# Performance work log

Measured on AMD Instinct MI355X. Metric: run time of the kernel, lower is better.

Reference implementation:

```python
import jax, jax.numpy as jnp
import numpy as np

B, N, K_OUT, NBASIS, NGLOBALS, H = 16, 2048, 128, 4, 2, 256
DIN = 1 + NBASIS + N + NGLOBALS  # norm + basis projections + all-pairs dots + globals
NEG_SLOPE = 0.01  # torch LeakyReLU default


def setup_inputs() -> dict:
    key = jax.random.key(0)
    ks = jax.random.split(key, 6)
    x = jax.random.uniform(ks[0], (B, N, 3), jnp.float32)      # positions -> dots >= 0
    u = jax.random.normal(ks[1], (B, NGLOBALS), jnp.float32)
    basis = jax.random.normal(ks[2], (B, NBASIS, 3), jnp.float32)
    def init_w(k, fan_in, fan_out):
        return jax.random.normal(k, (fan_in, fan_out), jnp.float32) / np.float32(np.sqrt(fan_in))
    W1 = init_w(ks[3], DIN, H); b1 = jnp.zeros((H,), jnp.float32)
    W2 = init_w(ks[4], H, H);   b2 = jnp.zeros((H,), jnp.float32)
    W3 = init_w(ks[5], H, K_OUT); b3 = jnp.zeros((K_OUT,), jnp.float32)
    return {"x": x, "u": u, "basis": basis,
            "W1": W1, "b1": b1, "W2": W2, "b2": b2, "W3": W3, "b3": b3}


def reference(x, u, basis, W1, b1, W2, b2, W3, b3):
    # per-vector norms: [B, N, 1]
    norms = jnp.linalg.norm(x, axis=-1, keepdims=True)
    # projections onto basis vectors: [B, N, NBASIS]
    proj = jnp.einsum('bid,bnd->bin', x, basis)
    # all-pairs sqrt of dot products: [B, N, N]
    dots = jnp.sqrt(jnp.einsum('bid,bjd->bij', x, x))
    # concat order matches original: globals first, then [norm, proj, dots]
    u_rep = jnp.broadcast_to(u[:, None, :], (B, N, NGLOBALS))
    scalars = jnp.concatenate([u_rep, norms, proj, dots], axis=-1)  # [B, N, DIN]
    # MLP (Linear -> LeakyReLU -> Linear -> LeakyReLU -> Linear)
    h = jax.nn.leaky_relu(scalars @ W1 + b1, NEG_SLOPE)
    h = jax.nn.leaky_relu(h @ W2 + b2, NEG_SLOPE)
    fk = h @ W3 + b3  # [B, N, K_OUT]
    # outer product with x followed by mean over input vecs, fused into one einsum
    # (avoids materializing the [B, N, K_OUT, 3] tensor)
    return jnp.einsum('bio,bid->bod', fk, x) / np.float32(N)  # [B, K_OUT, 3]
```

## Files before the change

kernel.cpp:

```cpp
#include <hip/hip_runtime.h>

typedef unsigned short u16;
typedef unsigned int   u32;

typedef __attribute__((ext_vector_type(8))) short short8;
typedef __attribute__((ext_vector_type(4))) float floatx4;

__device__ __forceinline__ u16 f2bf(float f) {
    u32 u = __float_as_uint(f);
    u = u + 0x7fffu + ((u >> 16) & 1u);
    return (u16)(u >> 16);
}

__device__ __forceinline__ u32 pack2bf(float s0, float s1) {
    u32 a = __float_as_uint(s0) + 0x8000u;
    u32 b = __float_as_uint(s1) + 0x8000u;
    return __builtin_amdgcn_perm(b, a, 0x07060302u);
}

__device__ __forceinline__ floatx4 mfma16(short8 a, short8 b, floatx4 c) {
    return __builtin_amdgcn_mfma_f32_16x16x32_bf16(a, b, c, 0, 0, 0);
}

__global__ void k_prep(const float* __restrict__ W1, const float* __restrict__ W2,
                       const float* __restrict__ W3, u16* __restrict__ W1frag,
                       u16* __restrict__ W2T, u16* __restrict__ W3T) {
    int idx = blockIdx.x * 256 + threadIdx.x;
    if (idx < 524288) {
        int kt = idx >> 13, r = idx & 8191;
        int t = r >> 5, jj = (r >> 3) & 3, ji = r & 7;
        int lane = t & 63, wv = t >> 6, lr = lane & 15, lq = lane >> 4;
        int n = wv * 64 + jj * 16 + lr;
        int k = kt * 32 + lq * 8 + ji;
        W1frag[idx] = f2bf(W1[(7 + k) * 256 + n]);
    } else if (idx < 589824) {
        int i = idx - 524288;
        int n = i >> 8, k = i & 255;
        W2T[i] = f2bf(W2[k * 256 + n]);
    } else if (idx < 622592) {
        int i = idx - 589824;
        int n = i >> 8, k = i & 255;
        W3T[i] = f2bf(W3[k * 128 + n]);
    }
}

__global__ __launch_bounds__(256, 2) void k_h1(
    const float* __restrict__ x, const float* __restrict__ u,
    const float* __restrict__ basis, const float* __restrict__ W1,
    const float* __restrict__ b1, const u16* __restrict__ W1frag,
    u16* __restrict__ h1) {
    __shared__ float4 xls4[1536];
    __shared__ u16 As[2][64][40];
    __shared__ float rowsml[64][6];
    __shared__ float colsml[256][6];

    const int t = threadIdx.x;
    const int b = blockIdx.y;
    const int i0 = blockIdx.x * 64;
    const int lane = t & 63, wv = t >> 6;
    const int lr = lane & 15, lq = lane >> 4;
    float* xls = (float*)xls4;

    {
        const float4* src = (const float4*)(x + b * 6144);
#pragma unroll
        for (int i = 0; i < 6; ++i) xls4[t + i * 256] = src[t + i * 256];
    }
    {
        int c = t;
        float u0 = u[b * 2 + 0], u1 = u[b * 2 + 1];
        colsml[c][0] = b1[c] + u0 * W1[c] + u1 * W1[256 + c];
        colsml[c][1] = W1[512 + c];
        colsml[c][2] = W1[768 + c];
        colsml[c][3] = W1[1024 + c];
        colsml[c][4] = W1[1280 + c];
        colsml[c][5] = W1[1536 + c];
    }
    __syncthreads();
    if (t < 64) {
        float xx = xls[(i0 + t) * 3], xy = xls[(i0 + t) * 3 + 1], xz = xls[(i0 + t) * 3 + 2];
        rowsml[t][0] = sqrtf(xx * xx + xy * xy + xz * xz);
#pragma unroll
        for (int p = 0; p < 4; ++p) {
            const float* bp = basis + (b * 4 + p) * 3;
            rowsml[t][1 + p] = xx * bp[0] + xy * bp[1] + xz * bp[2];
        }
    }
    const float ax = xls[(i0 + lane) * 3];
    const float ay = xls[(i0 + lane) * 3 + 1];
    const float az = xls[(i0 + lane) * 3 + 2];
    const int cbase = wv * 8;
    const u16* wf = W1frag + t * 32;

    auto gen_store = [&](int kt, int buf) {
        int q = kt * 24 + wv * 6;
        float4 q0 = xls4[q], q1 = xls4[q + 1], q2 = xls4[q + 2];
        float4 q3 = xls4[q + 3], q4 = xls4[q + 4], q5 = xls4[q + 5];
        float s0 = __builtin_amdgcn_sqrtf(ax * q0.x + ay * q0.y + az * q0.z);
        float s1 = __builtin_amdgcn_sqrtf(ax * q0.w + ay * q1.x + az * q1.y);
        float s2 = __builtin_amdgcn_sqrtf(ax * q1.z + ay * q1.w + az * q2.x);
        float s3 = __builtin_amdgcn_sqrtf(ax * q2.y + ay * q2.z + az * q2.w);
        float s4 = __builtin_amdgcn_sqrtf(ax * q3.x + ay * q3.y + az * q3.z);
        float s5 = __builtin_amdgcn_sqrtf(ax * q3.w + ay * q4.x + az * q4.y);
        float s6 = __builtin_amdgcn_sqrtf(ax * q4.z + ay * q4.w + az * q5.x);
        float s7 = __builtin_amdgcn_sqrtf(ax * q5.y + ay * q5.z + az * q5.w);
        uint4 dv;
        dv.x = pack2bf(s0, s1); dv.y = pack2bf(s2, s3);
        dv.z = pack2bf(s4, s5); dv.w = pack2bf(s6, s7);
        *(uint4*)&As[buf][lane][cbase] = dv;
    };

    floatx4 acc[4][4];
    const floatx4 zero = {0.f, 0.f, 0.f, 0.f};
#pragma unroll
    for (int i = 0; i < 4; ++i)
#pragma unroll
        for (int j = 0; j < 4; ++j) acc[i][j] = zero;

    short8 acur[4], bcur[4], bnxt[4];
    gen_store(0, 0);
#pragma unroll
    for (int j = 0; j < 4; ++j) bcur[j] = *(const short8*)(wf + j * 8);
    __syncthreads();
#pragma unroll
    for (int i = 0; i < 4; ++i) acur[i] = *(const short8*)&As[0][i * 16 + lr][lq * 8];

#pragma unroll 2
    for (int kt = 0; kt < 64; ++kt) {
        if (kt < 63) {
            const u16* wn = wf + (kt + 1) * 8192;
#pragma unroll
            for (int j = 0; j < 4; ++j) bnxt[j] = *(const short8*)(wn + j * 8);
            gen_store(kt + 1, (kt + 1) & 1);
        }
#pragma unroll
        for (int i = 0; i < 4; ++i)
#pragma unroll
            for (int j = 0; j < 4; ++j)
                acc[i][j] = mfma16(acur[i], bcur[j], acc[i][j]);
        __syncthreads();
        if (kt < 63) {
#pragma unroll
            for (int i = 0; i < 4; ++i)
                acur[i] = *(const short8*)&As[(kt + 1) & 1][i * 16 + lr][lq * 8];
#pragma unroll
            for (int j = 0; j < 4; ++j) bcur[j] = bnxt[j];
        }
    }

#pragma unroll
    for (int i = 0; i < 4; ++i) {
#pragma unroll
        for (int r = 0; r < 4; ++r) {
            int row = i * 16 + lq * 4 + r;
            float nrm = rowsml[row][0];
            float p0 = rowsml[row][1], p1 = rowsml[row][2];
            float p2 = rowsml[row][3], p3 = rowsml[row][4];
            u16* orow = h1 + (b * 2048 + i0 + row) * 256;
#pragma unroll
            for (int j = 0; j < 4; ++j) {
                int col = wv * 64 + j * 16 + lr;
                float v = acc[i][j][r] + colsml[col][0] + nrm * colsml[col][1] +
                          p0 * colsml[col][2] + p1 * colsml[col][3] +
                          p2 * colsml[col][4] + p3 * colsml[col][5];
                v = v > 0.f ? v : 0.01f * v;
                orow[col] = f2bf(v);
            }
        }
    }
}

__global__ __launch_bounds__(256, 2) void k_tail(
    const u16* __restrict__ h1, const u16* __restrict__ W2T,
    const float* __restrict__ b2, const u16* __restrict__ W3T,
    const float* __restrict__ b3, const float* __restrict__ x,
    float* __restrict__ accum) {
    __shared__ u16 As[64][40];
    __shared__ u16 Bs[256][40];
    __shared__ u16 h2s[64][264];
    __shared__ float colb2[256];
    __shared__ float colb3[128];
    __shared__ float xs[64][4];
    __shared__ float red[128][4];

    const int t = threadIdx.x;
    const int m0 = blockIdx.x * 64;
    const int b = m0 >> 11, i0 = m0 & 2047;
    const int lane = t & 63, wv = t >> 6;
    const int lr = lane & 15, lq = lane >> 4;

    colb2[t] = b2[t];
    if (t < 128) colb3[t] = b3[t];
    if (t < 64) {
        const float* xp = x + (b * 2048 + i0 + t) * 3;
        xs[t][0] = xp[0]; xs[t][1] = xp[1]; xs[t][2] = xp[2];
    }

    floatx4 acc[4][4];
    const floatx4 zero = {0.f, 0.f, 0.f, 0.f};
#pragma unroll
    for (int i = 0; i < 4; ++i)
#pragma unroll
        for (int j = 0; j < 4; ++j) acc[i][j] = zero;

    const int ar = t >> 2, ac = (t & 3) * 8;
    for (int kt = 0; kt < 8; ++kt) {
        *(uint4*)&As[ar][ac] = *(const uint4*)(h1 + (m0 + ar) * 256 + kt * 32 + ac);
        const u16* wsrc = W2T + t * 256 + kt * 32;
        *(uint4*)&Bs[t][0]  = *(const uint4*)(wsrc);
        *(uint4*)&Bs[t][8]  = *(const uint4*)(wsrc + 8);
        *(uint4*)&Bs[t][16] = *(const uint4*)(wsrc + 16);
        *(uint4*)&Bs[t][24] = *(const uint4*)(wsrc + 24);
        __syncthreads();
        short8 af[4], bf[4];
#pragma unroll
        for (int i = 0; i < 4; ++i) af[i] = *(const short8*)&As[i * 16 + lr][lq * 8];
#pragma unroll
        for (int j = 0; j < 4; ++j) bf[j] = *(const short8*)&Bs[wv * 64 + j * 16 + lr][lq * 8];
#pragma unroll
        for (int i = 0; i < 4; ++i)
#pragma unroll
            for (int j = 0; j < 4; ++j) acc[i][j] = mfma16(af[i], bf[j], acc[i][j]);
        __syncthreads();
    }
#pragma unroll
    for (int i = 0; i < 4; ++i)
#pragma unroll
        for (int r = 0; r < 4; ++r) {
            int row = i * 16 + lq * 4 + r;
#pragma unroll
            for (int j = 0; j < 4; ++j) {
                int col = wv * 64 + j * 16 + lr;
                float v = acc[i][j][r] + colb2[col];
                v = v > 0.f ? v : 0.01f * v;
                h2s[row][col] = f2bf(v);
            }
        }
    __syncthreads();

    floatx4 acc2[4][2];
#pragma unroll
    for (int i = 0; i < 4; ++i)
#pragma unroll
        for (int j = 0; j < 2; ++j) acc2[i][j] = zero;

    u16 (*Ws)[40] = (u16(*)[40])Bs;
    const int wr = t & 127, wseg = (t >> 7) * 16;
    for (int kt = 0; kt < 8; ++kt) {
        const u16* w3src = W3T + wr * 256 + kt * 32 + wseg;
        *(uint4*)&Ws[wr][wseg]     = *(const uint4*)(w3src);
        *(uint4*)&Ws[wr][wseg + 8] = *(const uint4*)(w3src + 8);
        __syncthreads();
        short8 af[4], bf[2];
#pragma unroll
        for (int i = 0; i < 4; ++i) af[i] = *(const short8*)&h2s[i * 16 + lr][kt * 32 + lq * 8];
#pragma unroll
        for (int j = 0; j < 2; ++j) bf[j] = *(const short8*)&Ws[wv * 32 + j * 16 + lr][lq * 8];
#pragma unroll
        for (int i = 0; i < 4; ++i)
#pragma unroll
            for (int j = 0; j < 2; ++j) acc2[i][j] = mfma16(af[i], bf[j], acc2[i][j]);
        __syncthreads();
    }

    float s[2][3];
#pragma unroll
    for (int j = 0; j < 2; ++j) { s[j][0] = 0.f; s[j][1] = 0.f; s[j][2] = 0.f; }
#pragma unroll
    for (int i = 0; i < 4; ++i)
#pragma unroll
        for (int r = 0; r < 4; ++r) {
            int row = i * 16 + lq * 4 + r;
            float x0 = xs[row][0], x1 = xs[row][1], x2 = xs[row][2];
#pragma unroll
            for (int j = 0; j < 2; ++j) {
                int col = wv * 32 + j * 16 + lr;
                float fk = acc2[i][j][r] + colb3[col];
                s[j][0] += fk * x0; s[j][1] += fk * x1; s[j][2] += fk * x2;
            }
        }
#pragma unroll
    for (int j = 0; j < 2; ++j)
#pragma unroll
        for (int d = 0; d < 3; ++d) {
            float v = s[j][d];
            v += __shfl_xor(v, 16);
            v += __shfl_xor(v, 32);
            if (lane < 16) red[wv * 32 + j * 16 + lane][d] = v;
        }
    __syncthreads();
    if (t < 128) {
#pragma unroll
        for (int d = 0; d < 3; ++d)
            atomicAdd(&accum[(b * 128 + t) * 3 + d], red[t][d]);
    }
}

__global__ void k_fin(const float* __restrict__ accum, float* __restrict__ out) {
    int idx = blockIdx.x * 256 + threadIdx.x;
    if (idx < 6144) out[idx] = accum[idx] * (1.0f / 2048.0f);
}

extern "C" void kernel_launch(void* const* d_in, const int* in_sizes, int n_in,
                              void* d_out, int out_size, void* d_ws, size_t ws_size,
                              hipStream_t stream) {
    const float* x     = (const float*)d_in[0];
    const float* u     = (const float*)d_in[1];
    const float* basis = (const float*)d_in[2];
    const float* W1    = (const float*)d_in[3];
    const float* b1    = (const float*)d_in[4];
    const float* W2    = (const float*)d_in[5];
    const float* b2    = (const float*)d_in[6];
    const float* W3    = (const float*)d_in[7];
    const float* b3    = (const float*)d_in[8];
    float* out = (float*)d_out;

    char* ws = (char*)d_ws;
    u16*  W1frag = (u16*)ws;
    u16*  W2T    = (u16*)(ws + 1048576);
    u16*  W3T    = (u16*)(ws + 1179648);
    u16*  h1     = (u16*)(ws + 1245184);
    float* accum = (float*)(ws + 18022400);

    hipMemsetAsync(accum, 0, 24576, stream);
    k_prep<<<2432, 256, 0, stream>>>(W1, W2, W3, W1frag, W2T, W3T);
    k_h1<<<dim3(32, 16), 256, 0, stream>>>(x, u, basis, W1, b1, W1frag, h1);
    k_tail<<<512, 256, 0, stream>>>(h1, W2T, b2, W3T, b3, x, accum);
    k_fin<<<24, 256, 0, stream>>>(accum, out);
}
```

Measured before the change: 145.0 us.

## Widen h1 to 8 waves with SoA x, fragment-packed W2/W3 loads in tail

Result: no change. 143.6 us (-1.0%).

```diff
diff --git a/kernel.cpp b/kernel.cpp
--- a/kernel.cpp
+++ b/kernel.cpp
@@ -5,6 +5,7 @@
 
 typedef __attribute__((ext_vector_type(8))) short short8;
 typedef __attribute__((ext_vector_type(4))) float floatx4;
+typedef __attribute__((ext_vector_type(2))) float v2f;
 
 __device__ __forceinline__ u16 f2bf(float f) {
     u32 u = __float_as_uint(f);
@@ -24,32 +25,34 @@
 
 __global__ void k_prep(const float* __restrict__ W1, const float* __restrict__ W2,
                        const float* __restrict__ W3, u16* __restrict__ W1frag,
-                       u16* __restrict__ W2T, u16* __restrict__ W3T) {
+                       u16* __restrict__ W2frag, u16* __restrict__ W3frag) {
     int idx = blockIdx.x * 256 + threadIdx.x;
     if (idx < 524288) {
         int kt = idx >> 13, r = idx & 8191;
+        int t = r >> 4, j = (r >> 3) & 1, ji = r & 7;
+        int lane = t & 63, w = t >> 6, lr = lane & 15, lq = lane >> 4;
+        W1frag[idx] = f2bf(W1[(7 + kt * 32 + lq * 8 + ji) * 256 + w * 32 + j * 16 + lr]);
+    } else if (idx < 589824) {
+        int i = idx - 524288;
+        int kt = i >> 13, r = i & 8191;
         int t = r >> 5, jj = (r >> 3) & 3, ji = r & 7;
         int lane = t & 63, wv = t >> 6, lr = lane & 15, lq = lane >> 4;
-        int n = wv * 64 + jj * 16 + lr;
-        int k = kt * 32 + lq * 8 + ji;
-        W1frag[idx] = f2bf(W1[(7 + k) * 256 + n]);
-    } else if (idx < 589824) {
-        int i = idx - 524288;
-        int n = i >> 8, k = i & 255;
-        W2T[i] = f2bf(W2[k * 256 + n]);
+        W2frag[i] = f2bf(W2[(kt * 32 + lq * 8 + ji) * 256 + wv * 64 + jj * 16 + lr]);
     } else if (idx < 622592) {
         int i = idx - 589824;
-        int n = i >> 8, k = i & 255;
-        W3T[i] = f2bf(W3[k * 128 + n]);
-    }
-}
-
-__global__ __launch_bounds__(256, 2) void k_h1(
+        int kt = i >> 12, r = i & 4095;
+        int t = r >> 4, j = (r >> 3) & 1, ji = r & 7;
+        int lane = t & 63, wv = t >> 6, lr = lane & 15, lq = lane >> 4;
+        W3frag[i] = f2bf(W3[(kt * 32 + lq * 8 + ji) * 128 + wv * 32 + j * 16 + lr]);
+    }
+}
+
+__global__ __launch_bounds__(512, 4) void k_h1(
     const float* __restrict__ x, const float* __restrict__ u,
     const float* __restrict__ basis, const float* __restrict__ W1,
     const float* __restrict__ b1, const u16* __restrict__ W1frag,
     u16* __restrict__ h1) {
-    __shared__ float4 xls4[1536];
+    __shared__ float xls[6144];
     __shared__ u16 As[2][64][40];
     __shared__ float rowsml[64][6];
     __shared__ float colsml[256][6];
@@ -57,16 +60,25 @@
     const int t = threadIdx.x;
     const int b = blockIdx.y;
     const int i0 = blockIdx.x * 64;
-    const int lane = t & 63, wv = t >> 6;
+    const int lane = t & 63, w = t >> 6;
     const int lr = lane & 15, lq = lane >> 4;
-    float* xls = (float*)xls4;
 
     {
         const float4* src = (const float4*)(x + b * 6144);
 #pragma unroll
-        for (int i = 0; i < 6; ++i) xls4[t + i * 256] = src[t + i * 256];
-    }
-    {
+        for (int kk = 0; kk < 3; ++kk) {
+            int q = t + kk * 512;
+            float4 v = src[q];
+            float vv[4] = {v.x, v.y, v.z, v.w};
+            int e = q * 4;
+#pragma unroll
+            for (int cc = 0; cc < 4; ++cc) {
+                int ee = e + cc;
+                xls[(ee % 3) * 2048 + ee / 3] = vv[cc];
+            }
+        }
+    }
+    if (t < 256) {
         int c = t;
         float u0 = u[b * 2 + 0], u1 = u[b * 2 + 1];
         colsml[c][0] = b1[c] + u0 * W1[c] + u1 * W1[256 + c];
@@ -78,7 +90,7 @@
     }
     __syncthreads();
     if (t < 64) {
-        float xx = xls[(i0 + t) * 3], xy = xls[(i0 + t) * 3 + 1], xz = xls[(i0 + t) * 3 + 2];
+        float xx = xls[i0 + t], xy = xls[2048 + i0 + t], xz = xls[4096 + i0 + t];
         rowsml[t][0] = sqrtf(xx * xx + xy * xy + xz * xz);
 #pragma unroll
         for (int p = 0; p < 4; ++p) {
@@ -86,41 +98,40 @@
             rowsml[t][1 + p] = xx * bp[0] + xy * bp[1] + xz * bp[2];
         }
     }
-    const float ax = xls[(i0 + lane) * 3];
-    const float ay = xls[(i0 + lane) * 3 + 1];
-    const float az = xls[(i0 + lane) * 3 + 2];
-    const int cbase = wv * 8;
-    const u16* wf = W1frag + t * 32;
+    const float ax = xls[i0 + lane];
+    const float ay = xls[2048 + i0 + lane];
+    const float az = xls[4096 + i0 + lane];
+    const u16* wf = W1frag + t * 16;
+    const float4* X4 = (const float4*)xls;
 
     auto gen_store = [&](int kt, int buf) {
-        int q = kt * 24 + wv * 6;
-        float4 q0 = xls4[q], q1 = xls4[q + 1], q2 = xls4[q + 2];
-        float4 q3 = xls4[q + 3], q4 = xls4[q + 4], q5 = xls4[q + 5];
-        float s0 = __builtin_amdgcn_sqrtf(ax * q0.x + ay * q0.y + az * q0.z);
-        float s1 = __builtin_amdgcn_sqrtf(ax * q0.w + ay * q1.x + az * q1.y);
-        float s2 = __builtin_amdgcn_sqrtf(ax * q1.z + ay * q1.w + az * q2.x);
-        float s3 = __builtin_amdgcn_sqrtf(ax * q2.y + ay * q2.z + az * q2.w);
-        float s4 = __builtin_amdgcn_sqrtf(ax * q3.x + ay * q3.y + az * q3.z);
-        float s5 = __builtin_amdgcn_sqrtf(ax * q3.w + ay * q4.x + az * q4.y);
-        float s6 = __builtin_amdgcn_sqrtf(ax * q4.z + ay * q4.w + az * q5.x);
-        float s7 = __builtin_amdgcn_sqrtf(ax * q5.y + ay * q5.z + az * q5.w);
-        uint4 dv;
-        dv.x = pack2bf(s0, s1); dv.y = pack2bf(s2, s3);
-        dv.z = pack2bf(s4, s5); dv.w = pack2bf(s6, s7);
-        *(uint4*)&As[buf][lane][cbase] = dv;
+        int q = kt * 8 + w;
+        float4 xv = X4[q], yv = X4[512 + q], zv = X4[1024 + q];
+        v2f xlo = {xv.x, xv.y}, xhi = {xv.z, xv.w};
+        v2f ylo = {yv.x, yv.y}, yhi = {yv.z, yv.w};
+        v2f zlo = {zv.x, zv.y}, zhi = {zv.z, zv.w};
+        v2f dlo = xlo * ax, dhi = xhi * ax;
+        dlo += ylo * ay; dhi += yhi * ay;
+        dlo += zlo * az; dhi += zhi * az;
+        float s0 = __builtin_amdgcn_sqrtf(dlo.x);
+        float s1 = __builtin_amdgcn_sqrtf(dlo.y);
+        float s2 = __builtin_amdgcn_sqrtf(dhi.x);
+        float s3 = __builtin_amdgcn_sqrtf(dhi.y);
+        uint2 dv; dv.x = pack2bf(s0, s1); dv.y = pack2bf(s2, s3);
+        *(uint2*)&As[buf][lane][w * 4] = dv;
     };
 
-    floatx4 acc[4][4];
+    floatx4 acc[4][2];
     const floatx4 zero = {0.f, 0.f, 0.f, 0.f};
 #pragma unroll
     for (int i = 0; i < 4; ++i)
 #pragma unroll
-        for (int j = 0; j < 4; ++j) acc[i][j] = zero;
-
-    short8 acur[4], bcur[4], bnxt[4];
+        for (int j = 0; j < 2; ++j) acc[i][j] = zero;
+
+    short8 acur[4], bcur[2], bnxt[2];
     gen_store(0, 0);
 #pragma unroll
-    for (int j = 0; j < 4; ++j) bcur[j] = *(const short8*)(wf + j * 8);
+    for (int j = 0; j < 2; ++j) bcur[j] = *(const short8*)(wf + j * 8);
     __syncthreads();
 #pragma unroll
     for (int i = 0; i < 4; ++i) acur[i] = *(const short8*)&As[0][i * 16 + lr][lq * 8];
@@ -130,13 +141,13 @@
         if (kt < 63) {
             const u16* wn = wf + (kt + 1) * 8192;
 #pragma unroll
-            for (int j = 0; j < 4; ++j) bnxt[j] = *(const short8*)(wn + j * 8);
+            for (int j = 0; j < 2; ++j) bnxt[j] = *(const short8*)(wn + j * 8);
             gen_store(kt + 1, (kt + 1) & 1);
         }
 #pragma unroll
         for (int i = 0; i < 4; ++i)
 #pragma unroll
-            for (int j = 0; j < 4; ++j)
+            for (int j = 0; j < 2; ++j)
                 acc[i][j] = mfma16(acur[i], bcur[j], acc[i][j]);
         __syncthreads();
         if (kt < 63) {
@@ -144,10 +155,14 @@
             for (int i = 0; i < 4; ++i)
                 acur[i] = *(const short8*)&As[(kt + 1) & 1][i * 16 + lr][lq * 8];
 #pragma unroll
-            for (int j = 0; j < 4; ++j) bcur[j] = bnxt[j];
-        }
-    }
-
+            for (int j = 0; j < 2; ++j) bcur[j] = bnxt[j];
+        }
+    }
+
+    const int c0 = w * 32 + lr, c1 = c0 + 16;
+    float c0v[6], c1v[6];
+#pragma unroll
+    for (int q = 0; q < 6; ++q) { c0v[q] = colsml[c0][q]; c1v[q] = colsml[c1][q]; }
 #pragma unroll
     for (int i = 0; i < 4; ++i) {
 #pragma unroll
@@ -157,26 +172,23 @@
             float p0 = rowsml[row][1], p1 = rowsml[row][2];
             float p2 = rowsml[row][3], p3 = rowsml[row][4];
             u16* orow = h1 + (b * 2048 + i0 + row) * 256;
-#pragma unroll
-            for (int j = 0; j < 4; ++j) {
-                int col = wv * 64 + j * 16 + lr;
-                float v = acc[i][j][r] + colsml[col][0] + nrm * colsml[col][1] +
-                          p0 * colsml[col][2] + p1 * colsml[col][3] +
-                          p2 * colsml[col][4] + p3 * colsml[col][5];
-                v = v > 0.f ? v : 0.01f * v;
-                orow[col] = f2bf(v);
-            }
+            float v0 = acc[i][0][r] + c0v[0] + nrm * c0v[1] +
+                       p0 * c0v[2] + p1 * c0v[3] + p2 * c0v[4] + p3 * c0v[5];
+            v0 = v0 > 0.f ? v0 : 0.01f * v0;
+            orow[c0] = f2bf(v0);
+            float v1 = acc[i][1][r] + c1v[0] + nrm * c1v[1] +
+                       p0 * c1v[2] + p1 * c1v[3] + p2 * c1v[4] + p3 * c1v[5];
+            v1 = v1 > 0.f ? v1 : 0.01f * v1;
+            orow[c1] = f2bf(v1);
         }
     }
 }
 
 __global__ __launch_bounds__(256, 2) void k_tail(
-    const u16* __restrict__ h1, const u16* __restrict__ W2T,
-    const float* __restrict__ b2, const u16* __restrict__ W3T,
+    const u16* __restrict__ h1, const u16* __restrict__ W2frag,
+    const float* __restrict__ b2, const u16* __restrict__ W3frag,
     const float* __restrict__ b3, const float* __restrict__ x,
     float* __restrict__ accum) {
-    __shared__ u16 As[64][40];
-    __shared__ u16 Bs[256][40];
     __shared__ u16 h2s[64][264];
     __shared__ float colb2[256];
     __shared__ float colb3[128];
@@ -203,25 +215,21 @@
 #pragma unroll
         for (int j = 0; j < 4; ++j) acc[i][j] = zero;
 
-    const int ar = t >> 2, ac = (t & 3) * 8;
+    const u16* hsrc = h1 + m0 * 256 + lr * 256 + lq * 8;
+    const u16* w2s = W2frag + t * 32;
+#pragma unroll 2
     for (int kt = 0; kt < 8; ++kt) {
-        *(uint4*)&As[ar][ac] = *(const uint4*)(h1 + (m0 + ar) * 256 + kt * 32 + ac);
-        const u16* wsrc = W2T + t * 256 + kt * 32;
-        *(uint4*)&Bs[t][0]  = *(const uint4*)(wsrc);
-        *(uint4*)&Bs[t][8]  = *(const uint4*)(wsrc + 8);
-        *(uint4*)&Bs[t][16] = *(const uint4*)(wsrc + 16);
-        *(uint4*)&Bs[t][24] = *(const uint4*)(wsrc + 24);
-        __syncthreads();
         short8 af[4], bf[4];
 #pragma unroll
-        for (int i = 0; i < 4; ++i) af[i] = *(const short8*)&As[i * 16 + lr][lq * 8];
-#pragma unroll
-        for (int j = 0; j < 4; ++j) bf[j] = *(const short8*)&Bs[wv * 64 + j * 16 + lr][lq * 8];
+        for (int i = 0; i < 4; ++i)
+            af[i] = *(const short8*)(hsrc + i * 4096 + kt * 32);
+#pragma unroll
+        for (int j = 0; j < 4; ++j)
+            bf[j] = *(const short8*)(w2s + kt * 8192 + j * 8);
 #pragma unroll
         for (int i = 0; i < 4; ++i)
 #pragma unroll
             for (int j = 0; j < 4; ++j) acc[i][j] = mfma16(af[i], bf[j], acc[i][j]);
-        __syncthreads();
     }
 #pragma unroll
     for (int i = 0; i < 4; ++i)
@@ -244,23 +252,20 @@
 #pragma unroll
         for (int j = 0; j < 2; ++j) acc2[i][j] = zero;
 
-    u16 (*Ws)[40] = (u16(*)[40])Bs;
-    const int wr = t & 127, wseg = (t >> 7) * 16;
+    const u16* w3s = W3frag + t * 16;
+#pragma unroll 2
     for (int kt = 0; kt < 8; ++kt) {
-        const u16* w3src = W3T + wr * 256 + kt * 32 + wseg;
-        *(uint4*)&Ws[wr][wseg]     = *(const uint4*)(w3src);
-        *(uint4*)&Ws[wr][wseg + 8] = *(const uint4*)(w3src + 8);
-        __syncthreads();
         short8 af[4], bf[2];
 #pragma unroll
-        for (int i = 0; i < 4; ++i) af[i] = *(const short8*)&h2s[i * 16 + lr][kt * 32 + lq * 8];
-#pragma unroll
-        for (int j = 0; j < 2; ++j) bf[j] = *(const short8*)&Ws[wv * 32 + j * 16 + lr][lq * 8];
+        for (int i = 0; i < 4; ++i)
+            af[i] = *(const short8*)&h2s[i * 16 + lr][kt * 32 + lq * 8];
+#pragma unroll
+        for (int j = 0; j < 2; ++j)
+            bf[j] = *(const short8*)(w3s + kt * 4096 + j * 8);
 #pragma unroll
         for (int i = 0; i < 4; ++i)
 #pragma unroll
             for (int j = 0; j < 2; ++j) acc2[i][j] = mfma16(af[i], bf[j], acc2[i][j]);
-        __syncthreads();
     }
 
     float s[2][3];
@@ -317,14 +322,14 @@
 
     char* ws = (char*)d_ws;
     u16*  W1frag = (u16*)ws;
-    u16*  W2T    = (u16*)(ws + 1048576);
-    u16*  W3T    = (u16*)(ws + 1179648);
+    u16*  W2frag = (u16*)(ws + 1048576);
+    u16*  W3frag = (u16*)(ws + 1179648);
     u16*  h1     = (u16*)(ws + 1245184);
     float* accum = (float*)(ws + 18022400);
 
     hipMemsetAsync(accum, 0, 24576, stream);
-    k_prep<<<2432, 256, 0, stream>>>(W1, W2, W3, W1frag, W2T, W3T);
-    k_h1<<<dim3(32, 16), 256, 0, stream>>>(x, u, basis, W1, b1, W1frag, h1);
-    k_tail<<<512, 256, 0, stream>>>(h1, W2T, b2, W3T, b3, x, accum);
+    k_prep<<<2432, 256, 0, stream>>>(W1, W2, W3, W1frag, W2frag, W3frag);
+    k_h1<<<dim3(32, 16), 512, 0, stream>>>(x, u, basis, W1, b1, W1frag, h1);
+    k_tail<<<512, 256, 0, stream>>>(h1, W2frag, b2, W3frag, b3, x, accum);
     k_fin<<<24, 256, 0, stream>>>(accum, out);
 }
```
